# Kernel tuning notes

Measured on AMD Instinct MI355X. Metric: run time of the kernel, lower is better.

The kernel has to match this reference:

```python
import jax, jax.numpy as jnp
import numpy as np

NPOINT = 2048
NSAMPLE = 16
LEAKY = 0.1
BN_EPS = 1e-5


def square_distance(src, dst):
    # src [B,S,3], dst [B,N,3] -> [B,S,N] squared euclidean
    d = -2.0 * jnp.einsum('bsc,bnc->bsn', src, dst)
    d = d + jnp.sum(src * src, -1)[:, :, None]
    d = d + jnp.sum(dst * dst, -1)[:, None, :]
    return d


def furthest_point_sample(xyz, npoint):
    # xyz [B,N,3] -> idx [B,npoint]; matches pointnet2 CUDA (seed = index 0)
    B, N, _ = xyz.shape

    def step(carry, _):
        dist, far = carry  # dist [B,N], far [B]
        centroid = jnp.take_along_axis(xyz, far[:, None, None], axis=1)  # [B,1,3]
        d = jnp.sum((xyz - centroid) ** 2, axis=-1)
        dist = jnp.minimum(dist, d)
        nxt = jnp.argmax(dist, axis=-1).astype(jnp.int32)
        return (dist, nxt), far

    init = (jnp.full((B, N), 1e10, xyz.dtype), jnp.zeros((B,), jnp.int32))
    _, idxs = jax.lax.scan(step, init, None, length=npoint)
    return idxs.T  # [B, npoint]


def _gather_nbrs(p, i):
    # p [N,C], i [S,K] -> [S,K,C]
    return p[i]


gather_group = jax.vmap(_gather_nbrs)


def conv_bn_lrelu(x, W, g, b):
    # x [B,Cin,S,K], W [Cout,Cin]; 1x1 conv + train-mode BatchNorm2d + LeakyReLU
    y = jnp.einsum('oc,bcsk->bosk', W, x)
    mean = jnp.mean(y, axis=(0, 2, 3), keepdims=True)
    var = jnp.var(y, axis=(0, 2, 3), keepdims=True)
    y = (y - mean) * jax.lax.rsqrt(var + BN_EPS)
    y = y * g[None, :, None, None] + b[None, :, None, None]
    return jnp.where(y > 0, y, LEAKY * y)


def setup_inputs() -> dict:
    key = jax.random.key(0)
    ks = jax.random.split(key, 5)
    B, N, D = 4, 8192, 64
    return {
        'xyz': jax.random.normal(ks[0], (B, 3, N), jnp.float32),
        'points': jax.random.normal(ks[1], (B, D, N), jnp.float32),
        'conv0_w': jax.random.normal(ks[2], (64, 67), jnp.float32) * 0.05,
        'conv1_w': jax.random.normal(ks[3], (64, 64), jnp.float32) * 0.05,
        'conv2_w': jax.random.normal(ks[4], (128, 64), jnp.float32) * 0.05,
        'bn0_g': jnp.ones((64,), jnp.float32),
        'bn0_b': jnp.zeros((64,), jnp.float32),
        'bn1_g': jnp.ones((64,), jnp.float32),
        'bn1_b': jnp.zeros((64,), jnp.float32),
        'bn2_g': jnp.ones((128,), jnp.float32),
        'bn2_b': jnp.zeros((128,), jnp.float32),
    }


def reference(xyz, points, conv0_w, conv1_w, conv2_w,
              bn0_g, bn0_b, bn1_g, bn1_b, bn2_g, bn2_b):
    xyz_t = jnp.transpose(xyz, (0, 2, 1))      # [B,N,3]
    pts_t = jnp.transpose(points, (0, 2, 1))   # [B,N,D]

    fps_idx = furthest_point_sample(xyz_t, NPOINT)                       # [B,S]
    new_xyz = jnp.take_along_axis(xyz_t, fps_idx[:, :, None], axis=1)    # [B,S,3]

    sqrd = square_distance(new_xyz, xyz_t)                               # [B,S,N]
    _, idx = jax.lax.top_k(-sqrd, NSAMPLE)                               # [B,S,K]

    grouped_xyz = gather_group(xyz_t, idx)                               # [B,S,K,3]
    grouped_norm = grouped_xyz - new_xyz[:, :, None, :]
    grouped_pts = gather_group(pts_t, idx)                               # [B,S,K,D]
    new_points = jnp.concatenate([grouped_norm, grouped_pts], axis=-1)   # [B,S,K,D+3]
    new_points = jnp.transpose(new_points, (0, 3, 1, 2))                 # [B,D+3,S,K]

    for W, g, b in ((conv0_w, bn0_g, bn0_b), (conv1_w, bn1_g, bn1_b),
                    (conv2_w, bn2_g, bn2_b)):
        new_points = conv_bn_lrelu(new_points, W, g, b)

    feat = jnp.max(new_points, axis=-1)                                  # [B,128,S]
    return jnp.transpose(new_xyz, (0, 2, 1)), feat, fps_idx
```

## Files before the change

kernel.cpp:

```cpp
#include <hip/hip_runtime.h>
#include <hip/hip_bf16.h>

#define BB 4
#define NP 8192
#define SS 2048
#define KK 16
#define DD 64
#define NN (BB*SS*KK)
#define HEATERS 128

typedef float vf2 __attribute__((ext_vector_type(2)));

__device__ __forceinline__ float wave_max_f32(float v) {
  int x;
  x = __builtin_amdgcn_update_dpp(0, __float_as_int(v), 0xB1, 0xF, 0xF, true);
  v = fmaxf(v, __int_as_float(x));
  x = __builtin_amdgcn_update_dpp(0, __float_as_int(v), 0x4E, 0xF, 0xF, true);
  v = fmaxf(v, __int_as_float(x));
  x = __builtin_amdgcn_update_dpp(0, __float_as_int(v), 0x141, 0xF, 0xF, true);
  v = fmaxf(v, __int_as_float(x));
  x = __builtin_amdgcn_update_dpp(0, __float_as_int(v), 0x140, 0xF, 0xF, true);
  v = fmaxf(v, __int_as_float(x));
  x = __builtin_amdgcn_ds_swizzle(__float_as_int(v), 0x401F);
  v = fmaxf(v, __int_as_float(x));
  v = fmaxf(v, __shfl_xor(v, 32, 64));
  return v;
}

__global__ __launch_bounds__(512) void fps_kernel(
    const float* __restrict__ xyz, float* __restrict__ newXyz,
    float* __restrict__ out, int* __restrict__ done)
{
  const int t = threadIdx.x;

  if (blockIdx.x >= BB) {
    float a0 = 1.0f, a1 = 1.1f, a2 = 1.2f, a3 = 1.3f;
    const float bm = 1.000001f, cm = 1e-7f;
    for (;;) {
      for (int k = 0; k < 1024; k++) {
        a0 = __builtin_fmaf(a0, bm, cm);
        a1 = __builtin_fmaf(a1, bm, cm);
        a2 = __builtin_fmaf(a2, bm, cm);
        a3 = __builtin_fmaf(a3, bm, cm);
      }
      if (__hip_atomic_load(done, __ATOMIC_RELAXED, __HIP_MEMORY_SCOPE_AGENT) >= BB)
        break;
    }
    if (a0 == 123.456f && a1 == 2.f && a2 == 3.f && a3 == 4.f)
      ((volatile int*)done)[1] = 1;
    return;
  }

  const int b = blockIdx.x;
  const float* xb = xyz + (size_t)b * 3 * NP;

  __shared__ float lx[NP], ly[NP], lz[NP];
  __shared__ int   wis[SS];
  __shared__ unsigned long long swin[3];

  vf2 px[8], py[8], pz[8], dist[8];
  const int i0 = t << 4;
#pragma unroll
  for (int h = 0; h < 8; h++) {
    int i = i0 + (h << 1);
    vf2 x = *(const vf2*)(xb + i);
    vf2 y = *(const vf2*)(xb + NP + i);
    vf2 z = *(const vf2*)(xb + 2 * NP + i);
    px[h] = x; py[h] = y; pz[h] = z;
    dist[h] = (vf2){1e10f, 1e10f};
    *(vf2*)(lx + i) = x; *(vf2*)(ly + i) = y; *(vf2*)(lz + i) = z;
  }
  if (t == 0) { wis[0] = 0; swin[0] = 0; swin[1] = 0; swin[2] = 0; }
  __syncthreads();

  float cx = lx[0], cy = ly[0], cz = lz[0];

  for (int it = 1; it < SS; ++it) {
    vf2 c2x = {cx, cx}, c2y = {cy, cy}, c2z = {cz, cz};
    vf2 lb = {-1.0f, -1.0f};
    {
#pragma clang fp contract(off)
#pragma unroll
      for (int h = 0; h < 8; h++) {
        vf2 dx = px[h] - c2x;
        vf2 dy = py[h] - c2y;
        vf2 dz = pz[h] - c2z;
        vf2 d  = (dx * dx + dy * dy) + dz * dz;
        vf2 dm = __builtin_elementwise_min(dist[h], d);
        dist[h] = dm;
        lb = __builtin_elementwise_max(lb, dm);
      }
    }
    float lbest = fmaxf(lb.x, lb.y);
    float Vw = wave_max_f32(lbest);
    int q = it % 3;
    if (lbest == Vw) {
      unsigned mi = 0u;
#pragma unroll
      for (int h = 7; h >= 0; h--) {
        unsigned base = (unsigned)(i0 + (h << 1));
        if (dist[h].y == Vw) mi = base + 1;
        if (dist[h].x == Vw) mi = base;
      }
      unsigned long long pk =
          ((unsigned long long)__float_as_uint(Vw) << 32) | (unsigned)(~mi);
      atomicMax(&swin[q], pk);
    }
    __syncthreads();
    unsigned long long pkf = swin[q];
    int ii = (int)(~((unsigned)pkf));
    if (t == 0) { wis[it] = ii; swin[(q + 2) % 3] = 0; }
    cx = lx[ii]; cy = ly[ii]; cz = lz[ii];
  }
  __syncthreads();

  float* outX = out;
  float* outI = out + 24576 + 1048576;
  for (int s = t; s < SS; s += 512) {
    int iw = wis[s];
    float x = lx[iw], y = ly[iw], z = lz[iw];
    size_t qq = (size_t)(b * SS + s);
    newXyz[qq * 3 + 0] = x;
    newXyz[qq * 3 + 1] = y;
    newXyz[qq * 3 + 2] = z;
    outX[(b * 3 + 0) * SS + s] = x;
    outX[(b * 3 + 1) * SS + s] = y;
    outX[(b * 3 + 2) * SS + s] = z;
    outI[b * SS + s] = (float)iw;
  }
  if (t == 0)
    __hip_atomic_fetch_add(done, 1, __ATOMIC_RELEASE, __HIP_MEMORY_SCOPE_AGENT);
}

__global__ __launch_bounds__(256) void knn_kernel(
    const float* __restrict__ xyz, const float* __restrict__ newXyz,
    int* __restrict__ knnIdx)
{
  const int t = threadIdx.x, w = t >> 6, l = t & 63;
  const int q = blockIdx.x * 4 + w;
  const int b = q >> 11;
  const float* xb = xyz + (size_t)b * 3 * NP;
  float qx = newXyz[q * 3], qy = newXyz[q * 3 + 1], qz = newXyz[q * 3 + 2];
  float ss = __fadd_rn(__fadd_rn(__fmul_rn(qx, qx), __fmul_rn(qy, qy)), __fmul_rn(qz, qz));
  float kd[16]; int ki[16];
#pragma unroll
  for (int j = 0; j < 16; j++) { kd[j] = __builtin_inff(); ki[j] = 0x7fffffff; }

  for (int m = 0; m < 128; m++) {
    int i = l + (m << 6);
    float x = xb[i], y = xb[NP + i], z = xb[2 * NP + i];
    float dot = __fadd_rn(__fadd_rn(__fmul_rn(x, qx), __fmul_rn(y, qy)), __fmul_rn(z, qz));
    float nn  = __fadd_rn(__fadd_rn(__fmul_rn(x, x), __fmul_rn(y, y)), __fmul_rn(z, z));
    float d   = __fadd_rn(__fadd_rn(__fmul_rn(-2.0f, dot), ss), nn);
    if (d < kd[15]) {
      kd[15] = d; ki[15] = i;
#pragma unroll
      for (int jj = 15; jj >= 1; jj--) {
        if (kd[jj] < kd[jj - 1]) {
          float td = kd[jj]; kd[jj] = kd[jj - 1]; kd[jj - 1] = td;
          int   ti = ki[jj]; ki[jj] = ki[jj - 1]; ki[jj - 1] = ti;
        }
      }
    }
  }

  __shared__ float sd[4 * 64 * 17];
  __shared__ int   sx[4 * 64 * 17];
  int base = (w * 64 + l) * 17;
#pragma unroll
  for (int j = 0; j < 16; j++) { sd[base + j] = kd[j]; sx[base + j] = ki[j]; }
  __syncthreads();

  int cur = 0; int outIdx = 0;
#pragma unroll 1
  for (int r = 0; r < 16; r++) {
    float hv = (cur < 16) ? sd[base + cur] : __builtin_inff();
    int   hi = (cur < 16) ? sx[base + cur] : 0x7fffffff;
    int   hl = l;
#pragma unroll
    for (int m2 = 1; m2 < 64; m2 <<= 1) {
      float ov = __shfl_xor(hv, m2, 64);
      int   oi = __shfl_xor(hi, m2, 64);
      int   ol = __shfl_xor(hl, m2, 64);
      if (ov < hv || (ov == hv && oi < hi)) { hv = ov; hi = oi; hl = ol; }
    }
    if (l == hl) cur++;
    if (l == r) outIdx = hi;
  }
  if (l < 16) knnIdx[q * 16 + l] = outIdx;
}

__global__ __launch_bounds__(256) void build_x0(
    const float* __restrict__ xyz, const float* __restrict__ points,
    const float* __restrict__ newXyz, const int* __restrict__ knnIdx,
    float* __restrict__ X)
{
  int n = blockIdx.x * 256 + threadIdx.x;
  int b = n >> 15;
  int q = n >> 4;
  int ip = knnIdx[n];
  const float* xb = xyz + (size_t)b * 3 * NP;
  X[(size_t)0 * NN + n] = xb[ip]          - newXyz[q * 3 + 0];
  X[(size_t)1 * NN + n] = xb[NP + ip]     - newXyz[q * 3 + 1];
  X[(size_t)2 * NN + n] = xb[2 * NP + ip] - newXyz[q * 3 + 2];
  const float* pb = points + (size_t)b * DD * NP;
#pragma unroll 8
  for (int d0 = 0; d0 < DD; d0++)
    X[(size_t)(3 + d0) * NN + n] = pb[(size_t)d0 * NP + ip];
}

template <int CIN, int COUT, bool BNIN>
__global__ __launch_bounds__(256) void conv_kernel(
    const float* __restrict__ X, const float* __restrict__ W,
    const float* __restrict__ ss, float* __restrict__ Y)
{
  __shared__ vf2 sss[CIN];
  if (BNIN) {
    for (int i = threadIdx.x; i < CIN; i += 256) sss[i] = ((const vf2*)ss)[i];
    __syncthreads();
  }
  int n = blockIdx.x * 256 + threadIdx.x;
  float x[CIN];
#pragma unroll
  for (int c = 0; c < CIN; c++) x[c] = X[(size_t)c * NN + n];
  if (BNIN) {
#pragma unroll
    for (int c = 0; c < CIN; c++) {
      vf2 p = sss[c];
      float v = fmaf(x[c], p.x, p.y);
      x[c] = v > 0.0f ? v : 0.1f * v;
    }
  }
#pragma unroll 1
  for (int o = 0; o < COUT; o += 4) {
    float a0 = 0.f, a1 = 0.f, a2 = 0.f, a3 = 0.f;
#pragma unroll
    for (int c = 0; c < CIN; c++) {
      float xv = x[c];
      a0 = fmaf(W[(o + 0) * CIN + c], xv, a0);
      a1 = fmaf(W[(o + 1) * CIN + c], xv, a1);
      a2 = fmaf(W[(o + 2) * CIN + c], xv, a2);
      a3 = fmaf(W[(o + 3) * CIN + c], xv, a3);
    }
    Y[(size_t)(o + 0) * NN + n] = a0;
    Y[(size_t)(o + 1) * NN + n] = a1;
    Y[(size_t)(o + 2) * NN + n] = a2;
    Y[(size_t)(o + 3) * NN + n] = a3;
  }
}

__global__ __launch_bounds__(256) void stats_kernel(
    const float* __restrict__ Y, float* __restrict__ stats)
{
  int c = blockIdx.y;
  int base = blockIdx.x * 4096 + threadIdx.x;
  const float* yc = Y + (size_t)c * NN;
  float s1 = 0.f, s2 = 0.f;
#pragma unroll
  for (int j = 0; j < 16; j++) {
    float v = yc[base + j * 256];
    s1 += v; s2 = fmaf(v, v, s2);
  }
#pragma unroll
  for (int m = 1; m < 64; m <<= 1) {
    s1 += __shfl_xor(s1, m, 64);
    s2 += __shfl_xor(s2, m, 64);
  }
  __shared__ float r1[4], r2[4];
  int w = threadIdx.x >> 6;
  if ((threadIdx.x & 63) == 0) { r1[w] = s1; r2[w] = s2; }
  __syncthreads();
  if (threadIdx.x == 0) {
    float t1 = r1[0] + r1[1] + r1[2] + r1[3];
    float t2 = r2[0] + r2[1] + r2[2] + r2[3];
    atomicAdd(&stats[c * 2], t1);
    atomicAdd(&stats[c * 2 + 1], t2);
  }
}

template <int C>
__global__ void finalize_kernel(const float* __restrict__ stats,
                                const float* __restrict__ g,
                                const float* __restrict__ bt,
                                float* __restrict__ ss)
{
  int c = threadIdx.x;
  if (c < C) {
    float mean = stats[c * 2] * (1.0f / NN);
    float var  = stats[c * 2 + 1] * (1.0f / NN) - mean * mean;
    float inv  = rsqrtf(var + 1e-5f);
    float sc = inv * g[c];
    float sh = bt[c] - mean * sc;
    ss[c * 2] = sc; ss[c * 2 + 1] = sh;
  }
}

__global__ __launch_bounds__(256) void maxk_kernel(
    const float* __restrict__ X, const float* __restrict__ ss,
    float* __restrict__ out)
{
  int m = blockIdx.x * 256 + threadIdx.x;
  int s = m & 2047;
  int o = (m >> 11) & 127;
  int b = m >> 18;
  float sc = ss[2 * o], sh = ss[2 * o + 1];
  const float4* p = (const float4*)(X + (size_t)o * NN + ((size_t)((b << 11) + s) << 4));
  float mx = -__builtin_inff();
#pragma unroll
  for (int j = 0; j < 4; j++) {
    float4 v4 = p[j];
    float a = fmaf(v4.x, sc, sh); a = a > 0.f ? a : 0.1f * a;
    float b2 = fmaf(v4.y, sc, sh); b2 = b2 > 0.f ? b2 : 0.1f * b2;
    float c = fmaf(v4.z, sc, sh); c = c > 0.f ? c : 0.1f * c;
    float d = fmaf(v4.w, sc, sh); d = d > 0.f ? d : 0.1f * d;
    mx = fmaxf(mx, fmaxf(fmaxf(a, b2), fmaxf(c, d)));
  }
  out[24576 + (size_t)((b << 7) + o) * SS + s] = mx;
}

extern "C" void kernel_launch(void* const* d_in, const int* in_sizes, int n_in,
                              void* d_out, int out_size, void* d_ws, size_t ws_size,
                              hipStream_t stream) {
  const float* xyz    = (const float*)d_in[0];
  const float* points = (const float*)d_in[1];
  const float* w0 = (const float*)d_in[2];
  const float* w1 = (const float*)d_in[3];
  const float* w2 = (const float*)d_in[4];
  const float* g0 = (const float*)d_in[5];
  const float* b0 = (const float*)d_in[6];
  const float* g1 = (const float*)d_in[7];
  const float* b1 = (const float*)d_in[8];
  const float* g2 = (const float*)d_in[9];
  const float* b2 = (const float*)d_in[10];
  float* out = (float*)d_out;

  float* wsf    = (float*)d_ws;
  float* newXyz = wsf;
  int*   knnIdx = (int*)(wsf + 24576);
  float* stats0 = wsf + 155648;
  float* stats1 = wsf + 155904;
  float* stats2 = wsf + 156160;
  float* ss0    = wsf + 156416;
  float* ss1    = wsf + 156672;
  float* ss2    = wsf + 156928;
  int*   done   = (int*)(wsf + 157440);
  float* Xa     = wsf + 160000;
  float* Xb     = wsf + 8941824;

  hipMemsetAsync(stats0, 0, 2048 * 4, stream);

  fps_kernel<<<BB + HEATERS, 512, 0, stream>>>(xyz, newXyz, out, done);
  knn_kernel<<<SS * BB / 4, 256, 0, stream>>>(xyz, newXyz, knnIdx);
  build_x0<<<NN / 256, 256, 0, stream>>>(xyz, points, newXyz, knnIdx, Xa);

  conv_kernel<67, 64, false><<<NN / 256, 256, 0, stream>>>(Xa, w0, nullptr, Xb);
  stats_kernel<<<dim3(32, 64), 256, 0, stream>>>(Xb, stats0);
  finalize_kernel<64><<<1, 128, 0, stream>>>(stats0, g0, b0, ss0);

  conv_kernel<64, 64, true><<<NN / 256, 256, 0, stream>>>(Xb, w1, ss0, Xa);
  stats_kernel<<<dim3(32, 64), 256, 0, stream>>>(Xa, stats1);
  finalize_kernel<64><<<1, 128, 0, stream>>>(stats1, g1, b1, ss1);

  conv_kernel<64, 128, true><<<NN / 256, 256, 0, stream>>>(Xa, w2, ss1, Xb);
  stats_kernel<<<dim3(32, 128), 256, 0, stream>>>(Xb, stats2);
  finalize_kernel<128><<<1, 128, 0, stream>>>(stats2, g2, b2, ss2);

  maxk_kernel<<<(BB * 128 * SS) / 256, 256, 0, stream>>>(Xb, ss2, out);
}
```

Measured before the change: 2.442 ms.

## Replace shared atomic argmax with per-wave slots and DPP cross-wave reduction in FPS

```diff
diff --git a/kernel.cpp b/kernel.cpp
--- a/kernel.cpp
+++ b/kernel.cpp
@@ -10,6 +10,12 @@
 #define HEATERS 128
 
 typedef float vf2 __attribute__((ext_vector_type(2)));
+
+#if defined(__has_builtin)
+#if __has_builtin(__builtin_amdgcn_permlane16_swap) && __has_builtin(__builtin_amdgcn_permlane32_swap)
+#define HAVE_PERMLANE_SWAP 1
+#endif
+#endif
 
 __device__ __forceinline__ float wave_max_f32(float v) {
   int x;
@@ -21,11 +27,24 @@
   v = fmaxf(v, __int_as_float(x));
   x = __builtin_amdgcn_update_dpp(0, __float_as_int(v), 0x140, 0xF, 0xF, true);
   v = fmaxf(v, __int_as_float(x));
+#ifdef HAVE_PERMLANE_SWAP
+  {
+    unsigned u = __float_as_uint(v);
+    auto r16 = __builtin_amdgcn_permlane16_swap(u, u, false, false);
+    v = fmaxf(__uint_as_float(r16[0]), __uint_as_float(r16[1]));
+    unsigned u2 = __float_as_uint(v);
+    auto r32 = __builtin_amdgcn_permlane32_swap(u2, u2, false, false);
+    v = fmaxf(__uint_as_float(r32[0]), __uint_as_float(r32[1]));
+  }
+#else
   x = __builtin_amdgcn_ds_swizzle(__float_as_int(v), 0x401F);
   v = fmaxf(v, __int_as_float(x));
   v = fmaxf(v, __shfl_xor(v, 32, 64));
+#endif
   return v;
 }
+
+#define DPP_U(x, ctrl) ((unsigned)__builtin_amdgcn_update_dpp(0, (int)(x), ctrl, 0xF, 0xF, true))
 
 __global__ __launch_bounds__(512) void fps_kernel(
     const float* __restrict__ xyz, float* __restrict__ newXyz,
@@ -52,11 +71,13 @@
   }
 
   const int b = blockIdx.x;
+  const int l = t & 63, w = t >> 6;
   const float* xb = xyz + (size_t)b * 3 * NP;
 
   __shared__ float lx[NP], ly[NP], lz[NP];
   __shared__ int   wis[SS];
-  __shared__ unsigned long long swin[3];
+  __shared__ uint4 slot[2][8];
+  __shared__ unsigned slotz[2][8];
 
   vf2 px[8], py[8], pz[8], dist[8];
   const int i0 = t << 4;
@@ -70,14 +91,15 @@
     dist[h] = (vf2){1e10f, 1e10f};
     *(vf2*)(lx + i) = x; *(vf2*)(ly + i) = y; *(vf2*)(lz + i) = z;
   }
-  if (t == 0) { wis[0] = 0; swin[0] = 0; swin[1] = 0; swin[2] = 0; }
+  if (t == 0) wis[0] = 0;
   __syncthreads();
 
   float cx = lx[0], cy = ly[0], cz = lz[0];
 
   for (int it = 1; it < SS; ++it) {
+    const int p = it & 1;
     vf2 c2x = {cx, cx}, c2y = {cy, cy}, c2z = {cz, cz};
-    vf2 lb = {-1.0f, -1.0f};
+    vf2 lb0 = {-1.0f, -1.0f}, lb1 = {-1.0f, -1.0f};
     {
 #pragma clang fp contract(off)
 #pragma unroll
@@ -88,29 +110,61 @@
         vf2 d  = (dx * dx + dy * dy) + dz * dz;
         vf2 dm = __builtin_elementwise_min(dist[h], d);
         dist[h] = dm;
-        lb = __builtin_elementwise_max(lb, dm);
+        if (h & 1) lb1 = __builtin_elementwise_max(lb1, dm);
+        else       lb0 = __builtin_elementwise_max(lb0, dm);
       }
     }
-    float lbest = fmaxf(lb.x, lb.y);
+    float lbest = fmaxf(fmaxf(lb0.x, lb0.y), fmaxf(lb1.x, lb1.y));
     float Vw = wave_max_f32(lbest);
-    int q = it % 3;
-    if (lbest == Vw) {
-      unsigned mi = 0u;
+
+    unsigned long long bal = __ballot(lbest == Vw);
+    if (bal != 0ull && l == (int)__builtin_ctzll(bal)) {
+      unsigned mi = 0u; float wx = 0.f, wy = 0.f, wz = 0.f;
 #pragma unroll
       for (int h = 7; h >= 0; h--) {
         unsigned base = (unsigned)(i0 + (h << 1));
-        if (dist[h].y == Vw) mi = base + 1;
-        if (dist[h].x == Vw) mi = base;
+        if (dist[h].y == Vw) { mi = base + 1; wx = px[h].y; wy = py[h].y; wz = pz[h].y; }
+        if (dist[h].x == Vw) { mi = base;     wx = px[h].x; wy = py[h].x; wz = pz[h].x; }
       }
-      unsigned long long pk =
-          ((unsigned long long)__float_as_uint(Vw) << 32) | (unsigned)(~mi);
-      atomicMax(&swin[q], pk);
+      uint4 sv;
+      sv.x = ~mi;
+      sv.y = __float_as_uint(Vw);
+      sv.z = __float_as_uint(wx);
+      sv.w = __float_as_uint(wy);
+      slot[p][w] = sv;
+      slotz[p][w] = __float_as_uint(wz);
     }
     __syncthreads();
-    unsigned long long pkf = swin[q];
-    int ii = (int)(~((unsigned)pkf));
-    if (t == 0) { wis[it] = ii; swin[(q + 2) % 3] = 0; }
-    cx = lx[ii]; cy = ly[ii]; cz = lz[ii];
+
+    uint4 sv = slot[p][l & 7];
+    unsigned kLo = sv.x, kHi = sv.y, vxu = sv.z, vyu = sv.w;
+    unsigned vzu = slotz[p][l & 7];
+    {
+      unsigned oL = DPP_U(kLo, 0xB1), oH = DPP_U(kHi, 0xB1);
+      unsigned oX = DPP_U(vxu, 0xB1), oY = DPP_U(vyu, 0xB1), oZ = DPP_U(vzu, 0xB1);
+      bool tk = (oH > kHi) || (oH == kHi && oL > kLo);
+      kLo = tk ? oL : kLo; kHi = tk ? oH : kHi;
+      vxu = tk ? oX : vxu; vyu = tk ? oY : vyu; vzu = tk ? oZ : vzu;
+    }
+    {
+      unsigned oL = DPP_U(kLo, 0x4E), oH = DPP_U(kHi, 0x4E);
+      unsigned oX = DPP_U(vxu, 0x4E), oY = DPP_U(vyu, 0x4E), oZ = DPP_U(vzu, 0x4E);
+      bool tk = (oH > kHi) || (oH == kHi && oL > kLo);
+      kLo = tk ? oL : kLo; kHi = tk ? oH : kHi;
+      vxu = tk ? oX : vxu; vyu = tk ? oY : vyu; vzu = tk ? oZ : vzu;
+    }
+    {
+      unsigned oL = DPP_U(kLo, 0x141), oH = DPP_U(kHi, 0x141);
+      unsigned oX = DPP_U(vxu, 0x141), oY = DPP_U(vyu, 0x141), oZ = DPP_U(vzu, 0x141);
+      bool tk = (oH > kHi) || (oH == kHi && oL > kLo);
+      kLo = tk ? oL : kLo; kHi = tk ? oH : kHi;
+      vxu = tk ? oX : vxu; vyu = tk ? oY : vyu; vzu = tk ? oZ : vzu;
+    }
+    int ii = (int)(~kLo);
+    if (t == 0) wis[it] = ii;
+    cx = __uint_as_float(vxu);
+    cy = __uint_as_float(vyu);
+    cz = __uint_as_float(vzu);
   }
   __syncthreads();
 
```

Result: slower. 2.877 ms (+17.8%).
